# Optimization experiments

Measured on AMD Instinct MI355X. Metric: run time of the kernel, lower is better.

The kernel has to match this reference:

```python
import jax, jax.numpy as jnp
import numpy as np

B, L, H, D, TXT = 128, 512, 336, 256, 768
K, S, EMB = 16, 4, 128
H_SCALE = 0.15
EPS, ITERS = 0.05, 30
ALPHA, BETA = 1.0, 0.5
GW, TAU = 0.5, 0.07
LMB_MSE, LMB_COT, LMB_DELTA, LMB_ENT, LMB_TV = 1.0, 0.1, 0.1, 0.01, 0.01


def setup_inputs() -> dict:
    key = jax.random.key(0)
    ks = jax.random.split(key, 12)
    def xav(k, shape):
        return jax.random.normal(k, shape, jnp.float32) / np.sqrt(shape[0]).astype(np.float32)
    inp = {}
    inp['y_res'] = jax.random.normal(ks[0], (B, H, D), jnp.float32)
    inp['text_emb'] = jax.random.normal(ks[1], (B, TXT), jnp.float32)
    inp['enc_out'] = jax.random.normal(ks[2], (B, L, D), jnp.float32)
    inp['y_future'] = jax.random.normal(ks[3], (B, H, D), jnp.float32)
    inp['perm'] = jax.random.permutation(ks[4], EMB)
    inp['W_t2k'] = xav(ks[5], (TXT, K * (3 + S))); inp['b_t2k'] = jnp.zeros((K * (3 + S),), jnp.float32)
    inp['W_kemb'] = xav(ks[6], (H, EMB)); inp['b_kemb'] = jnp.zeros((EMB,), jnp.float32)
    inp['W_tir'] = xav(ks[7], (1, D)); inp['b_tir'] = jnp.zeros((D,), jnp.float32)
    inp['var_proj'] = jnp.ones((D,), jnp.float32)
    inp['W_g1'] = xav(ks[8], (2 * D + TXT, 512)); inp['b_g1'] = jnp.zeros((512,), jnp.float32)
    inp['W_g2'] = xav(ks[9], (512, D)); inp['b_g2'] = jnp.zeros((D,), jnp.float32)
    inp['W_fp'] = xav(ks[10], (3 * D, EMB)); inp['b_fp'] = jnp.zeros((EMB,), jnp.float32)
    return inp


def _text2kernels(text_emb, W, b):
    # text -> K temporal kernels: mixture of S shape bases with learned mu/sigma/amp
    raw = (text_emb @ W + b).reshape(-1, K, 3 + S)
    mu = jax.nn.sigmoid(raw[..., 0])                       # [B,K] center in [0,1]
    sig = jax.nn.softplus(raw[..., 1]) * H_SCALE + 1e-3     # [B,K] width
    amp = jax.nn.softplus(raw[..., 2])                      # [B,K]
    shape_w = jax.nn.softmax(raw[..., 3:], axis=-1)         # [B,K,S]
    t = (jnp.arange(H, dtype=text_emb.dtype) + 0.5) / H     # [H]
    z = (t[None, None, :] - mu[..., None]) / sig[..., None]  # [B,K,H]
    az = jnp.abs(z)
    in_supp = (az <= 1.0).astype(z.dtype)
    basis = jnp.stack([
        jnp.exp(-0.5 * z * z),
        jnp.exp(-az),
        jnp.maximum(1.0 - az, 0.0),
        0.5 * (1.0 + jnp.cos(jnp.pi * jnp.clip(z, -1.0, 1.0))) * in_supp,
    ], axis=-1)                                             # [B,K,H,S]
    kappa = amp[..., None] * jnp.einsum('bkhs,bks->bkh', basis, shape_w)
    return kappa, mu, shape_w


def _future_proj(y, W, b):
    # concat(y, first diff, second diff) -> linear, in_dim = 3*D
    d1 = jnp.diff(y, axis=1, prepend=y[:, :1])
    d2 = jnp.diff(d1, axis=1, prepend=d1[:, :1])
    return jnp.concatenate([y, d1, d2], axis=-1) @ W + b    # [B,H,EMB]


def _l2n(x):
    return x / (jnp.linalg.norm(x, axis=-1, keepdims=True) + 1e-8)


def _causal_cost(k_emb, f_pos, mu):
    cossim = jnp.einsum('bkd,bhd->bkh', _l2n(k_emb), _l2n(f_pos))
    t = (jnp.arange(H, dtype=k_emb.dtype) + 0.5) / H
    causal = jnp.maximum(mu[:, :, None] - t[None, None, :], 0.0)  # effect-before-cause penalty
    return ALPHA * (1.0 - cossim) + BETA * causal            # [B,K,H]


def _sinkhorn(C, r, c):
    Kmat = jnp.exp(-C / EPS)
    def body(i, uv):
        u, v = uv
        u = r / (jnp.einsum('bkh,bh->bk', Kmat, v) + 1e-9)
        v = c / (jnp.einsum('bkh,bk->bh', Kmat, u) + 1e-9)
        return (u, v)
    u, v = jax.lax.fori_loop(0, ITERS, body, (jnp.ones_like(r), jnp.ones_like(c)))
    return u[:, :, None] * Kmat * v[:, None, :]              # [B,K,H]


def _delta_contrastive(k_emb, f_pos, Pi, negatives):
    w = Pi / (jnp.sum(Pi, axis=-1, keepdims=True) + 1e-9)    # transport-weighted aggregation
    kn = _l2n(k_emb)
    def sim(f):
        return jnp.einsum('bkd,bkd->bk', kn, _l2n(jnp.einsum('bkh,bhd->bkd', w, f)))
    logits = jnp.stack([sim(f_pos)] + [sim(f) for f in negatives], axis=-1) / TAU  # [B,K,1+neg]
    return -jnp.mean(jax.nn.log_softmax(logits, axis=-1)[..., 0])


def reference(y_res, text_emb, enc_out, y_future, perm, W_t2k, b_t2k, W_kemb, b_kemb,
              W_tir, b_tir, var_proj, W_g1, b_g1, W_g2, b_g2, W_fp, b_fp):
    # --- text-induced response ---
    kappa, mu, shape_w = _text2kernels(text_emb, W_t2k, b_t2k)   # [B,K,H]
    y_tir_scalar = kappa.sum(axis=1)                             # [B,H]
    # --- gated fusion ---
    y_tir = (y_tir_scalar[..., None] @ W_tir + b_tir) * var_proj[None, None, :]  # [B,H,D]
    ts_global = enc_out.mean(axis=1)                             # [B,D]
    gate_in = jnp.concatenate([ts_global, text_emb, jnp.broadcast_to(var_proj[None, :], (y_res.shape[0], D))], axis=-1)
    gate = jax.nn.sigmoid(jax.nn.relu(gate_in @ W_g1 + b_g1) @ W_g2 + b_g2)[:, None, :]  # [B,1,D]
    y_hat = y_res + GW * gate * (y_tir - y_res)
    # --- aux losses ---
    k_emb = kappa @ W_kemb + b_kemb                              # [B,K,EMB]
    f_pos = _future_proj(y_future, W_fp, b_fp)                   # [B,H,EMB]
    C = _causal_cost(k_emb, f_pos, mu)
    r = jax.lax.stop_gradient(kappa.sum(-1) + 1e-6)
    r = r / r.sum(axis=-1, keepdims=True)
    c = jnp.full((C.shape[0], C.shape[2]), 1.0 / C.shape[2], C.dtype)
    Pi = _sinkhorn(C, r, c)
    shift = max(1, H // 6)
    f_neg1 = jnp.roll(f_pos, shift, axis=1)
    f_neg2 = f_pos[..., perm]
    loss_delta = _delta_contrastive(k_emb, f_pos, Pi, [f_neg1, f_neg2])
    loss_cot = jnp.mean(jnp.sum(C * Pi, axis=(1, 2)))
    sw = jnp.maximum(shape_w, 1e-8)
    loss_ent = -jnp.mean(jnp.sum(sw * jnp.log(sw), axis=-1))
    loss_tv = jnp.mean(jnp.abs(mu[:, 1:] - mu[:, :-1]))
    loss_mse = jnp.mean((y_hat - y_future) ** 2)
    return (LMB_MSE * loss_mse + LMB_COT * loss_cot + LMB_DELTA * loss_delta
            + LMB_ENT * loss_ent + LMB_TV * loss_tv)
```

## Files before the change

### kernel.cpp

```cpp
#include <hip/hip_runtime.h>
#include <math.h>

#define Bn   128
#define Ln   512
#define Hn   336
#define Dn   256
#define TXTn 768
#define Kn   16
#define EMBn 128
#define SHIFT 56
#define MSEB 1024
#define FROWS 48
#define FTILES 7
#define ASTRIDE 776

typedef __attribute__((ext_vector_type(8))) short short8;
typedef __attribute__((ext_vector_type(4))) float floatx4;

__device__ __forceinline__ float softplusf(float x){
  return fmaxf(x, 0.f) + log1pf(expf(-fabsf(x)));
}
__device__ __forceinline__ unsigned short f2bf(float x){
  unsigned int u = __float_as_uint(x);
  unsigned int r = (u + 0x7fffu + ((u >> 16) & 1u)) >> 16;
  return (unsigned short)r;
}
__device__ __forceinline__ float rcpf(float x){ return __builtin_amdgcn_rcpf(x); }
__device__ __forceinline__ float wsum(float x){
  x += __shfl_xor(x, 1);  x += __shfl_xor(x, 2);  x += __shfl_xor(x, 4);
  x += __shfl_xor(x, 8);  x += __shfl_xor(x, 16); x += __shfl_xor(x, 32);
  return x;
}

__global__ __launch_bounds__(256) void k_fused1(
    const float* __restrict__ text, const float* __restrict__ W, const float* __restrict__ bb,
    float* __restrict__ mu_o, float* __restrict__ kapT, float* __restrict__ rr_o,
    float* __restrict__ ytirs, float* __restrict__ part_ent, float* __restrict__ part_tv){
  int b = blockIdx.x, t = threadIdx.x;
  __shared__ float kapS[Kn*Hn];
  __shared__ float musL[Kn], sigL[Kn], ampL[Kn], shwL[Kn*4], entS[Kn], rrS[Kn];
  __shared__ float red[256];
  __shared__ float comb[112];
  __shared__ float totS;
  {
    int o = t & 127, half = t >> 7;
    if (o < 112){
      const float* tb = text + (size_t)b*TXTn + half*384;
      const float* Wb = W + (size_t)half*384*112 + o;
      float a0=0.f, a1=0.f, a2=0.f, a3=0.f;
      for (int i = 0; i < 384; i += 4){
        float4 x = *(const float4*)(tb + i);
        a0 += x.x*Wb[(i+0)*112]; a1 += x.y*Wb[(i+1)*112];
        a2 += x.z*Wb[(i+2)*112]; a3 += x.w*Wb[(i+3)*112];
      }
      red[half*112 + o] = (a0 + a1) + (a2 + a3);
    }
  }
  __syncthreads();
  if (t < 112) comb[t] = red[t] + red[112 + t] + bb[t];
  __syncthreads();
  if (t < Kn){
    float r0 = comb[t*7+0], r1 = comb[t*7+1], r2 = comb[t*7+2];
    float mu  = 1.f/(1.f+expf(-r0));
    float sig = softplusf(r1)*0.15f + 1e-3f;
    float amp = softplusf(r2);
    float s0 = comb[t*7+3], s1 = comb[t*7+4], s2 = comb[t*7+5], s3 = comb[t*7+6];
    float m = fmaxf(fmaxf(s0,s1), fmaxf(s2,s3));
    float e0 = expf(s0-m), e1 = expf(s1-m), e2 = expf(s2-m), e3 = expf(s3-m);
    float inv = 1.f/(e0+e1+e2+e3);
    float w0 = e0*inv, w1 = e1*inv, w2 = e2*inv, w3 = e3*inv;
    musL[t] = mu; sigL[t] = sig; ampL[t] = amp;
    shwL[t*4+0] = w0; shwL[t*4+1] = w1; shwL[t*4+2] = w2; shwL[t*4+3] = w3;
    mu_o[b*Kn + t] = mu;
    float ent = 0.f, sw;
    sw = fmaxf(w0,1e-8f); ent += sw*logf(sw);
    sw = fmaxf(w1,1e-8f); ent += sw*logf(sw);
    sw = fmaxf(w2,1e-8f); ent += sw*logf(sw);
    sw = fmaxf(w3,1e-8f); ent += sw*logf(sw);
    entS[t] = ent;
  }
  __syncthreads();
  for (int p = t; p < Kn*Hn; p += 256){
    int k = p/Hn, h = p - k*Hn;
    float mu = musL[k], sig = sigL[k], amp = ampL[k];
    float w0 = shwL[k*4+0], w1 = shwL[k*4+1], w2 = shwL[k*4+2], w3 = shwL[k*4+3];
    float tt = (h + 0.5f)/(float)Hn;
    float z  = (tt - mu)/sig;
    float az = fabsf(z);
    float b0 = expf(-0.5f*z*z);
    float b1 = expf(-az);
    float b2 = fmaxf(1.f-az, 0.f);
    float zc = fminf(fmaxf(z,-1.f),1.f);
    float b3 = (az <= 1.f) ? 0.5f*(1.f+cosf(3.14159265358979f*zc)) : 0.f;
    kapS[p] = amp*(w0*b0 + w1*b1 + w2*b2 + w3*b3);
  }
  __syncthreads();
  for (int q = t; q < Kn*Hn; q += 256){
    int h = q >> 4, k = q & 15;
    kapT[((size_t)b*Hn + h)*Kn + k] = kapS[k*Hn + h];
  }
  {
    int k = t >> 4, j16 = t & 15;
    float s = 0.f;
    for (int h = j16; h < Hn; h += 16) s += kapS[k*Hn + h];
    red[t] = s;
  }
  __syncthreads();
  if (t < Kn){
    float s = 0.f;
    for (int j = 0; j < 16; ++j) s += red[t*16 + j];
    rrS[t] = s + 1e-6f;
  }
  __syncthreads();
  if (t == 0){
    float tot = 0.f, tv = 0.f, es = 0.f;
    for (int k = 0; k < Kn; ++k) tot += rrS[k];
    for (int k = 1; k < Kn; ++k) tv += fabsf(musL[k]-musL[k-1]);
    for (int k = 0; k < Kn; ++k) es += entS[k];
    totS = tot; part_tv[b] = tv; part_ent[b] = es;
  }
  __syncthreads();
  if (t < Kn) rr_o[b*Kn + t] = rrS[t]/totS;
  for (int h = t; h < Hn; h += 256){
    float s = 0.f;
    #pragma unroll
    for (int k = 0; k < Kn; ++k) s += kapS[k*Hn + h];
    ytirs[b*Hn + h] = s;
  }
}

__global__ __launch_bounds__(128) void k_kemb1(const float* __restrict__ kapT,
    const float* __restrict__ W, float* __restrict__ kp){
  int blk = blockIdx.x;
  int b = blk >> 3, oc = blk & 7;
  int e = threadIdx.x;
  float acc[Kn];
  #pragma unroll
  for (int k = 0; k < Kn; ++k) acc[k] = 0.f;
  const float* kb = kapT + (size_t)b*Hn*Kn;
  int h0 = oc*42, h1 = h0 + 42;
  for (int h = h0; h < h1; ++h){
    float wv = W[h*EMBn + e];
    const float4* kr = (const float4*)(kb + h*Kn);
    float4 c0 = kr[0], c1 = kr[1], c2 = kr[2], c3 = kr[3];
    acc[0]  += c0.x*wv; acc[1]  += c0.y*wv; acc[2]  += c0.z*wv; acc[3]  += c0.w*wv;
    acc[4]  += c1.x*wv; acc[5]  += c1.y*wv; acc[6]  += c1.z*wv; acc[7]  += c1.w*wv;
    acc[8]  += c2.x*wv; acc[9]  += c2.y*wv; acc[10] += c2.z*wv; acc[11] += c2.w*wv;
    acc[12] += c3.x*wv; acc[13] += c3.y*wv; acc[14] += c3.z*wv; acc[15] += c3.w*wv;
  }
  float* kpb = kp + ((size_t)blk*Kn)*EMBn + e;
  #pragma unroll
  for (int k = 0; k < Kn; ++k) kpb[(size_t)k*EMBn] = acc[k];
}

__global__ __launch_bounds__(256) void k_kemb2(const float* __restrict__ kp,
    const float* __restrict__ bb, float* __restrict__ kn_o){
  int b = blockIdx.x, t = threadIdx.x;
  __shared__ float kS[Kn*EMBn];
  __shared__ float r2[256];
  __shared__ float invS[Kn];
  for (int j = t; j < Kn*EMBn; j += 256){
    int e = j & 127;
    float s = bb[e];
    const float* p = kp + (size_t)b*8*Kn*EMBn + j;
    #pragma unroll
    for (int oc = 0; oc < 8; ++oc) s += p[(size_t)oc*Kn*EMBn];
    kS[j] = s;
  }
  __syncthreads();
  {
    int k = t & 15, g = t >> 4;
    float s = 0.f;
    for (int e = g; e < EMBn; e += 16){ float v = kS[k*EMBn + e]; s += v*v; }
    r2[g*Kn + k] = s;
  }
  __syncthreads();
  if (t < Kn){
    float s = 0.f;
    for (int g = 0; g < 16; ++g) s += r2[g*Kn + t];
    invS[t] = 1.f/(sqrtf(s) + 1e-8f);
  }
  __syncthreads();
  for (int j = t; j < Kn*EMBn; j += 256)
    kn_o[(size_t)b*Kn*EMBn + j] = kS[j]*invS[j >> 7];
}

__global__ void k_wprep(const float* __restrict__ W, unsigned short* __restrict__ Bsw){
  int tid = blockIdx.x*256 + threadIdx.x;
  int k = tid >> 7, n = tid & 127;
  int kt = k >> 5, kr = k & 31, quad = kr >> 3, j = kr & 7;
  int c = n >> 4, ln = n & 15;
  int lane = quad*16 + ln;
  int dst = ((kt*8 + c)*64 + lane)*8 + j;
  Bsw[dst] = f2bf(W[k*128 + n]);
}

__global__ __launch_bounds__(256) void k_encmean(const float* __restrict__ enc,
                                                 float* __restrict__ psum){
  int blk = blockIdx.x;
  int b = blk >> 3, p = blk & 7;
  int t = threadIdx.x;
  int d4 = t & 63, rg = t >> 6;
  const float4* e4 = (const float4*)(enc + (size_t)b*Ln*Dn);
  float4 s = make_float4(0.f,0.f,0.f,0.f);
  for (int l = p + 8*rg; l < Ln; l += 32){
    float4 v = e4[(size_t)l*64 + d4];
    s.x += v.x; s.y += v.y; s.z += v.z; s.w += v.w;
  }
  __shared__ float4 red[256];
  red[t] = s;
  __syncthreads();
  if (rg == 0){
    float4 o = red[d4];
    #pragma unroll
    for (int r = 1; r < 4; ++r){
      float4 v = red[r*64 + d4];
      o.x += v.x; o.y += v.y; o.z += v.z; o.w += v.w;
    }
    ((float4*)(psum + ((size_t)b*8 + p)*Dn))[d4] = o;
  }
}

__global__ __launch_bounds__(256) void k_gmlp1(const float* __restrict__ psum,
    const float* __restrict__ text, const float* __restrict__ vp,
    const float* __restrict__ W1, float* __restrict__ hidp){
  int bt = blockIdx.x >> 5, hc = (blockIdx.x >> 2) & 7, ks = blockIdx.x & 3;
  int t = threadIdx.x;
  __shared__ float inS[4][320];
  for (int j = t; j < 4*320; j += 256){
    int bi = j / 320, jj = j - bi*320;
    int gi = ks*320 + jj;
    int b = bt*4 + bi;
    float vsl;
    if (gi < Dn){
      float s = 0.f;
      for (int p = 0; p < 8; ++p) s += psum[((size_t)b*8 + p)*Dn + gi];
      vsl = s * (1.f/(float)Ln);
    } else if (gi < Dn + TXTn){
      vsl = text[(size_t)b*TXTn + (gi - Dn)];
    } else {
      vsl = vp[gi - Dn - TXTn];
    }
    inS[bi][jj] = vsl;
  }
  __syncthreads();
  int h = t & 63, bi = t >> 6;
  int hidx = hc*64 + h;
  const float* Wb = W1 + (size_t)(ks*320)*512 + hidx;
  float a0 = 0.f, a1 = 0.f, a2 = 0.f, a3 = 0.f;
  const float4* in4 = (const float4*)inS[bi];
  for (int i = 0; i < 320; i += 4){
    float4 x = in4[i >> 2];
    a0 += x.x*Wb[(size_t)(i+0)*512]; a1 += x.y*Wb[(size_t)(i+1)*512];
    a2 += x.z*Wb[(size_t)(i+2)*512]; a3 += x.w*Wb[(size_t)(i+3)*512];
  }
  hidp[((size_t)ks*Bn + bt*4 + bi)*512 + hidx] = (a0 + a1) + (a2 + a3);
}

__global__ __launch_bounds__(256) void k_gmlp2(const float* __restrict__ hidp,
    const float* __restrict__ b1, const float* __restrict__ W2,
    const float* __restrict__ b2, float* __restrict__ gate_o){
  int bt = blockIdx.x >> 3, dc = blockIdx.x & 7;
  int t = threadIdx.x;
  __shared__ float hS[4][512];
  __shared__ float pS[8][4][32];
  for (int j = t; j < 4*512; j += 256){
    int bi = j >> 9, i = j & 511;
    size_t bidx = (size_t)(bt*4 + bi)*512 + i;
    float s = hidp[bidx] + hidp[(size_t)Bn*512 + bidx]
            + hidp[(size_t)2*Bn*512 + bidx] + hidp[(size_t)3*Bn*512 + bidx];
    hS[bi][i] = fmaxf(s + b1[i], 0.f);
  }
  __syncthreads();
  {
    int dl = t & 31, ig = t >> 5;
    int d  = dc*32 + dl;
    float a0=0.f, a1=0.f, a2=0.f, a3=0.f;
    int i0 = ig*64;
    for (int i = i0; i < i0 + 64; ++i){
      float wv = W2[(size_t)i*Dn + d];
      a0 += hS[0][i]*wv; a1 += hS[1][i]*wv;
      a2 += hS[2][i]*wv; a3 += hS[3][i]*wv;
    }
    pS[ig][0][dl] = a0; pS[ig][1][dl] = a1;
    pS[ig][2][dl] = a2; pS[ig][3][dl] = a3;
  }
  __syncthreads();
  if (t < 128){
    int bi = t >> 5, dl = t & 31;
    float s = 0.f;
    #pragma unroll
    for (int g = 0; g < 8; ++g) s += pS[g][bi][dl];
    s += b2[dc*32 + dl];
    gate_o[(size_t)(bt*4 + bi)*Dn + dc*32 + dl] = 1.f/(1.f + expf(-s));
  }
}

__global__ __launch_bounds__(256) void k_fposm(const float* __restrict__ yf,
    const unsigned short* __restrict__ Bsw, const float* __restrict__ bb,
    float* __restrict__ fpos, float* __restrict__ finv){
  int b = blockIdx.x / FTILES, tile = blockIdx.x % FTILES;
  int t = threadIdx.x;
  int h0 = tile*FROWS;
  __shared__ unsigned short yS[FROWS*ASTRIDE];
  __shared__ float rsq[4][FROWS];
  const float* yb = yf + (size_t)b*Hn*Dn;

  #pragma unroll
  for (int u = 0; u < 12; ++u){
    int unit = t + 256*u;
    int r = unit >> 6, d4 = unit & 63;
    int h = h0 + r;
    int hm1 = h-1 < 0 ? 0 : h-1;
    int hm2 = h-2 < 0 ? 0 : h-2;
    float4 y   = *(const float4*)(yb + (size_t)h  *Dn + d4*4);
    float4 ym1 = *(const float4*)(yb + (size_t)hm1*Dn + d4*4);
    float4 ym2 = *(const float4*)(yb + (size_t)hm2*Dn + d4*4);
    float4 d1 = make_float4(y.x-ym1.x, y.y-ym1.y, y.z-ym1.z, y.w-ym1.w);
    float4 d2 = make_float4(y.x-2.f*ym1.x+ym2.x, y.y-2.f*ym1.y+ym2.y,
                            y.z-2.f*ym1.z+ym2.z, y.w-2.f*ym1.w+ym2.w);
    union { unsigned short u16[4]; uint2 v; } p;
    unsigned short* base = &yS[r*ASTRIDE + d4*4];
    p.u16[0]=f2bf(y.x);  p.u16[1]=f2bf(y.y);  p.u16[2]=f2bf(y.z);  p.u16[3]=f2bf(y.w);
    *(uint2*)(base)        = p.v;
    p.u16[0]=f2bf(d1.x); p.u16[1]=f2bf(d1.y); p.u16[2]=f2bf(d1.z); p.u16[3]=f2bf(d1.w);
    *(uint2*)(base + 256)  = p.v;
    p.u16[0]=f2bf(d2.x); p.u16[1]=f2bf(d2.y); p.u16[2]=f2bf(d2.z); p.u16[3]=f2bf(d2.w);
    *(uint2*)(base + 512)  = p.v;
  }
  __syncthreads();

  int wv   = __builtin_amdgcn_readfirstlane(t >> 6);
  int lane = t & 63, quad = lane >> 4, ln = lane & 15;
  int c0 = wv*2;
  floatx4 acc[3][2];
  #pragma unroll
  for (int i = 0; i < 3; ++i){
    acc[i][0] = (floatx4){0.f,0.f,0.f,0.f};
    acc[i][1] = (floatx4){0.f,0.f,0.f,0.f};
  }
  #pragma unroll
  for (int kt = 0; kt < 24; ++kt){
    int aoff = kt*32 + quad*8;
    short8 a0 = *(const short8*)&yS[( 0 + ln)*ASTRIDE + aoff];
    short8 a1 = *(const short8*)&yS[(16 + ln)*ASTRIDE + aoff];
    short8 a2 = *(const short8*)&yS[(32 + ln)*ASTRIDE + aoff];
    short8 b0 = *(const short8*)&Bsw[((kt*8 + c0  )*64 + lane)*8];
    short8 b1 = *(const short8*)&Bsw[((kt*8 + c0+1)*64 + lane)*8];
    acc[0][0] = __builtin_amdgcn_mfma_f32_16x16x32_bf16(a0, b0, acc[0][0], 0, 0, 0);
    acc[0][1] = __builtin_amdgcn_mfma_f32_16x16x32_bf16(a0, b1, acc[0][1], 0, 0, 0);
    acc[1][0] = __builtin_amdgcn_mfma_f32_16x16x32_bf16(a1, b0, acc[1][0], 0, 0, 0);
    acc[1][1] = __builtin_amdgcn_mfma_f32_16x16x32_bf16(a1, b1, acc[1][1], 0, 0, 0);
    acc[2][0] = __builtin_amdgcn_mfma_f32_16x16x32_bf16(a2, b0, acc[2][0], 0, 0, 0);
    acc[2][1] = __builtin_amdgcn_mfma_f32_16x16x32_bf16(a2, b1, acc[2][1], 0, 0, 0);
  }

  float bias0 = bb[c0*16 + ln], bias1 = bb[(c0+1)*16 + ln];
  #pragma unroll
  for (int rt = 0; rt < 3; ++rt){
    #pragma unroll
    for (int reg = 0; reg < 4; ++reg){
      int lrow = rt*16 + quad*4 + reg;
      size_t row = (size_t)b*Hn + h0 + lrow;
      float v0 = acc[rt][0][reg] + bias0;
      float v1 = acc[rt][1][reg] + bias1;
      fpos[row*EMBn + c0*16 + ln]     = v0;
      fpos[row*EMBn + (c0+1)*16 + ln] = v1;
      float sq = v0*v0 + v1*v1;
      sq += __shfl_xor(sq, 1); sq += __shfl_xor(sq, 2);
      sq += __shfl_xor(sq, 4); sq += __shfl_xor(sq, 8);
      if (ln == 0) rsq[wv][lrow] = sq;
    }
  }
  __syncthreads();
  if (t < FROWS){
    float s = rsq[0][t] + rsq[1][t] + rsq[2][t] + rsq[3][t];
    finv[(size_t)b*Hn + h0 + t] = 1.f/(sqrtf(s) + 1e-8f);
  }
}

__global__ void k_mse(const float* __restrict__ yres, const float* __restrict__ yfut,
                      const float* __restrict__ gate, const float* __restrict__ ytirs,
                      const float* __restrict__ Wt, const float* __restrict__ bt,
                      const float* __restrict__ vp, float* __restrict__ part_mse){
  const long long total = (long long)Bn*Hn*Dn;
  long long tid = blockIdx.x*(long long)blockDim.x + threadIdx.x;
  long long nth = gridDim.x*(long long)blockDim.x;
  float part = 0.f;
  for (long long i4 = tid; i4*4 < total; i4 += nth){
    long long base = i4*4;
    int b = (int)(base/((long long)Hn*Dn));
    int rem = (int)(base - (long long)b*Hn*Dn);
    int h = rem/Dn, d = rem - h*Dn;
    float4 yr = *(const float4*)(yres + base);
    float4 yv = *(const float4*)(yfut + base);
    float4 g  = *(const float4*)(gate + (size_t)b*Dn + d);
    float4 wt = *(const float4*)(Wt + d);
    float4 bv = *(const float4*)(bt + d);
    float4 vv = *(const float4*)(vp + d);
    float ys = ytirs[b*Hn + h];
    float yt, yh, e;
    yt = (ys*wt.x + bv.x)*vv.x; yh = yr.x + 0.5f*g.x*(yt-yr.x); e = yh-yv.x; part += e*e;
    yt = (ys*wt.y + bv.y)*vv.y; yh = yr.y + 0.5f*g.y*(yt-yr.y); e = yh-yv.y; part += e*e;
    yt = (ys*wt.z + bv.z)*vv.z; yh = yr.z + 0.5f*g.z*(yt-yr.z); e = yh-yv.z; part += e*e;
    yt = (ys*wt.w + bv.w)*vv.w; yh = yr.w + 0.5f*g.w*(yt-yr.w); e = yh-yv.w; part += e*e;
  }
  __shared__ float red[256];
  red[threadIdx.x] = part; __syncthreads();
  for (int s = 128; s > 0; s >>= 1){
    if (threadIdx.x < s) red[threadIdx.x] += red[threadIdx.x + s];
    __syncthreads();
  }
  if (threadIdx.x == 0) part_mse[blockIdx.x] = red[0];
}

__global__ __launch_bounds__(256) void k_cost(const float* __restrict__ kn,
    const float* __restrict__ fpos, const float* __restrict__ finv,
    const float* __restrict__ mu_i, float* __restrict__ Km_g){
  int b = blockIdx.x >> 2, q = blockIdx.x & 3;
  int t = threadIdx.x;
  __shared__ float knS[Kn*132];
  __shared__ float musS[Kn];
  for (int j = t; j < Kn*EMBn; j += 256){
    int k = j >> 7, e = j & 127;
    knS[k*132 + e] = kn[(size_t)b*Kn*EMBn + j];
  }
  if (t < Kn) musS[t] = mu_i[b*Kn + t];
  __syncthreads();
  const int H0 = q*84;
  for (int p = t; p < Kn*84; p += 256){
    int k = p & 15, h = H0 + (p >> 4);
    const float4* f4 = (const float4*)(fpos + ((size_t)b*Hn + h)*EMBn);
    const float4* k4 = (const float4*)(knS + k*132);
    float s = 0.f;
    #pragma unroll 8
    for (int i = 0; i < EMBn/4; ++i){
      float4 a = k4[i], f = f4[i];
      s += a.x*f.x + a.y*f.y + a.z*f.z + a.w*f.w;
    }
    float cs = s*finv[b*Hn + h];
    float th = (h + 0.5f)/(float)Hn;
    float c  = (1.f - cs) + 0.5f*fmaxf(musS[k] - th, 0.f);
    Km_g[(size_t)b*Kn*Hn + k*Hn + h] = expf(-20.f*c);
  }
}

__global__ __launch_bounds__(128) void k_sink1w(const float* __restrict__ rr,
    float* KmwT, float* __restrict__ part_cot){
  int b = blockIdx.x, t = threadIdx.x;
  int l = t & 63;
  float* Kb = KmwT + (size_t)b*Kn*Hn;
  int ks = ((l&1)<<3) | ((l&2)<<1) | ((l&4)>>1) | ((l&8)>>3);
  __shared__ float ws[128];
  float km[16][3];
  #pragma unroll
  for (int m = 0; m < 16; ++m){
    const float* rowp = Kb + (size_t)(ks ^ m)*Hn;
    #pragma unroll
    for (int c = 0; c < 3; ++c){
      int h = 128*c + t;
      km[m][c] = (h < Hn) ? rowp[h] : 0.f;
    }
  }
  float rrl = rr[b*Kn + ks];
  float v[3];
  v[0] = 1.f; v[1] = 1.f; v[2] = 1.f;
  float w[16];
  for (int it = 0; it < 30; ++it){
    float p[16];
    #pragma unroll
    for (int m = 0; m < 16; ++m)
      p[m] = km[m][0]*v[0] + km[m][1]*v[1] + km[m][2]*v[2];
    #pragma unroll
    for (int m = 0; m < 8; ++m) p[m] += __shfl_xor(p[m+8], 1);
    #pragma unroll
    for (int m = 0; m < 4; ++m) p[m] += __shfl_xor(p[m+4], 2);
    #pragma unroll
    for (int m = 0; m < 2; ++m) p[m] += __shfl_xor(p[m+2], 4);
    p[0] += __shfl_xor(p[1], 8);
    p[0] += __shfl_xor(p[0], 16);
    p[0] += __shfl_xor(p[0], 32);
    ws[t] = p[0];
    __syncthreads();
    float ptot = ws[l] + ws[64 + l];
    __syncthreads();
    float ul = rrl * rcpf(ptot + 1e-9f);
    w[0] = ul;
    w[1] = __shfl_xor(w[0], 8);
    w[2] = __shfl_xor(w[0], 4); w[3] = __shfl_xor(w[1], 4);
    #pragma unroll
    for (int j = 0; j < 4; ++j) w[4+j] = __shfl_xor(w[j], 2);
    #pragma unroll
    for (int j = 0; j < 8; ++j) w[8+j] = __shfl_xor(w[j], 1);
    #pragma unroll
    for (int c = 0; c < 3; ++c){
      float s0 = 0.f, s1 = 0.f;
      #pragma unroll
      for (int m = 0; m < 8; ++m){ s0 += km[m][c]*w[m]; s1 += km[m+8][c]*w[m+8]; }
      v[c] = (1.f/(float)Hn) * rcpf(s0 + s1 + 1e-9f);
    }
  }
  float q[16];
  #pragma unroll
  for (int m = 0; m < 16; ++m)
    q[m] = km[m][0]*v[0] + km[m][1]*v[1] + km[m][2]*v[2];
  #pragma unroll
  for (int m = 0; m < 8; ++m) q[m] += __shfl_xor(q[m+8], 1);
  #pragma unroll
  for (int m = 0; m < 4; ++m) q[m] += __shfl_xor(q[m+4], 2);
  #pragma unroll
  for (int m = 0; m < 2; ++m) q[m] += __shfl_xor(q[m+2], 4);
  q[0] += __shfl_xor(q[1], 8);
  q[0] += __shfl_xor(q[0], 16);
  q[0] += __shfl_xor(q[0], 32);
  ws[t] = q[0];
  __syncthreads();
  float qtot = ws[l] + ws[64 + l];
  __syncthreads();
  float tt[16];
  tt[0] = qtot;
  tt[1] = __shfl_xor(tt[0], 8);
  tt[2] = __shfl_xor(tt[0], 4); tt[3] = __shfl_xor(tt[1], 4);
  #pragma unroll
  for (int j = 0; j < 4; ++j) tt[4+j] = __shfl_xor(tt[j], 2);
  #pragma unroll
  for (int j = 0; j < 8; ++j) tt[8+j] = __shfl_xor(tt[j], 1);
  float cot = 0.f;
  #pragma unroll
  for (int m = 0; m < 16; ++m){
    float rsinv = rcpf(w[m]*tt[m] + 1e-9f);
    float* rowp = Kb + (size_t)(ks ^ m)*Hn;
    #pragma unroll
    for (int c = 0; c < 3; ++c){
      int h = 128*c + t;
      if (h < Hn){
        float Pi = w[m]*km[m][c]*v[c];
        cot += (-0.05f)*logf(km[m][c])*Pi;
        rowp[h] = Pi*rsinv;
      }
    }
  }
  cot = wsum(cot);
  ws[t] = cot;
  __syncthreads();
  if (t == 0) part_cot[b] = ws[0] + ws[64];
}

__global__ __launch_bounds__(256) void k_agg(const float* __restrict__ kn,
    const float* __restrict__ fpos, const float* __restrict__ wT,
    const int* __restrict__ perm, float* __restrict__ part_del4){
  int b = blockIdx.x >> 2, kg = blockIdx.x & 3;
  int t = threadIdx.x;
  __shared__ float wTl[Hn*4];
  __shared__ float apH[2][4*EMBn];
  __shared__ float a1H[2][4*EMBn];
  __shared__ int permS[EMBn];
  __shared__ float redW[4];
  if (t < EMBn) permS[t] = perm[t];
  for (int j = t; j < 4*Hn; j += 256){
    int k = j & 3, h = j >> 2;
    wTl[h*4 + k] = wT[(size_t)b*Kn*Hn + (size_t)(kg*4 + k)*Hn + h];
  }
  __syncthreads();

  {
    int e = t & 127, jh = t >> 7;
    float ap[4], a1[4];
    #pragma unroll
    for (int j = 0; j < 4; ++j){ ap[j] = 0.f; a1[j] = 0.f; }
    const float* fb = fpos + (size_t)b*Hn*EMBn + e;
    int hh0 = jh*168, hh1 = hh0 + 168;
    for (int h = hh0; h < hh1; ++h){
      float fv = fb[(size_t)h*EMBn];
      int h1 = h + SHIFT; if (h1 >= Hn) h1 -= Hn;
      float4 wA = *(const float4*)&wTl[h *4];
      float4 wB = *(const float4*)&wTl[h1*4];
      ap[0] += wA.x*fv; ap[1] += wA.y*fv; ap[2] += wA.z*fv; ap[3] += wA.w*fv;
      a1[0] += wB.x*fv; a1[1] += wB.y*fv; a1[2] += wB.z*fv; a1[3] += wB.w*fv;
    }
    #pragma unroll
    for (int j = 0; j < 4; ++j){
      apH[jh][j*EMBn + e] = ap[j];
      a1H[jh][j*EMBn + e] = a1[j];
    }
  }
  __syncthreads();
  for (int j = t; j < 4*EMBn; j += 256){
    apH[0][j] += apH[1][j];
    a1H[0][j] += a1H[1][j];
  }
  __syncthreads();

  int wave = t >> 6, lane = t & 63;
  {
    int kl = wave;
    int k  = kg*4 + kl;
    float sp = 0.f, s1 = 0.f, s2 = 0.f, np = 0.f, n1 = 0.f;
    for (int e = lane; e < EMBn; e += 64){
      float kne = kn[((size_t)b*Kn + k)*EMBn + e];
      float a  = apH[0][kl*EMBn + e];
      float c1 = a1H[0][kl*EMBn + e];
      sp += kne*a; s1 += kne*c1;
      s2 += kne*apH[0][kl*EMBn + permS[e]];
      np += a*a; n1 += c1*c1;
    }
    for (int o = 32; o; o >>= 1){
      sp += __shfl_down(sp, o); s1 += __shfl_down(s1, o); s2 += __shfl_down(s2, o);
      np += __shfl_down(np, o); n1 += __shfl_down(n1, o);
    }
    if (lane == 0){
      float ip  = 1.f/(sqrtf(np) + 1e-8f);
      float i1v = 1.f/(sqrtf(n1) + 1e-8f);
      const float ti = 1.f/0.07f;
      float l0 = sp*ip*ti, l1 = s1*i1v*ti, l2 = s2*ip*ti;
      float m = fmaxf(l0, fmaxf(l1, l2));
      float lse = m + logf(expf(l0-m) + expf(l1-m) + expf(l2-m));
      redW[wave] = lse - l0;
    }
  }
  __syncthreads();
  if (t == 0) part_del4[(size_t)b*4 + kg] = redW[0] + redW[1] + redW[2] + redW[3];
}

__global__ void k_final(const float* __restrict__ part_mse, const float* __restrict__ part_cot,
                        const float* __restrict__ part_del4, const float* __restrict__ part_ent,
                        const float* __restrict__ part_tv, float* __restrict__ out){
  int t = threadIdx.x;
  __shared__ double sred[256];
  double m = 0.0;
  for (int i = t; i < MSEB; i += 256) m += (double)part_mse[i];
  double o4 = 0.0;
  if (t < Bn){
    double del = (double)part_del4[4*t] + (double)part_del4[4*t + 1]
               + (double)part_del4[4*t + 2] + (double)part_del4[4*t + 3];
    o4 = 0.1*(double)part_cot[t] + (0.1/(double)Kn)*del
       - (0.01/(double)Kn)*(double)part_ent[t] + (0.01/(double)(Kn-1))*(double)part_tv[t];
  }
  sred[t] = m/((double)Bn*Hn*Dn) + o4/(double)Bn;
  __syncthreads();
  for (int s = 128; s > 0; s >>= 1){ if (t < s) sred[t] += sred[t+s]; __syncthreads(); }
  if (t == 0) out[0] = (float)sred[0];
}

extern "C" void kernel_launch(void* const* d_in, const int* in_sizes, int n_in,
                              void* d_out, int out_size, void* d_ws, size_t ws_size,
                              hipStream_t stream) {
  const float* y_res  = (const float*)d_in[0];
  const float* text   = (const float*)d_in[1];
  const float* enc    = (const float*)d_in[2];
  const float* yfut   = (const float*)d_in[3];
  const int*   perm   = (const int*)  d_in[4];
  const float* W_t2k  = (const float*)d_in[5];
  const float* b_t2k  = (const float*)d_in[6];
  const float* W_kemb = (const float*)d_in[7];
  const float* b_kemb = (const float*)d_in[8];
  const float* W_tir  = (const float*)d_in[9];
  const float* b_tir  = (const float*)d_in[10];
  const float* vproj  = (const float*)d_in[11];
  const float* W_g1   = (const float*)d_in[12];
  const float* b_g1   = (const float*)d_in[13];
  const float* W_g2   = (const float*)d_in[14];
  const float* b_g2   = (const float*)d_in[15];
  const float* W_fp   = (const float*)d_in[16];
  const float* b_fp   = (const float*)d_in[17];

  float* F = (float*)d_ws;
  float* mu_w   = F;
  float* rr_w   = F + 2048;
  float* ytr_w  = F + 4096;
  float* kapT_w = F + 47104;
  float* kn_w   = F + 735232;
  float* gate_w = F + 997376;
  float* fp_w   = F + 1030144;
  float* fi_w   = F + 6535168;
  float* pmse_w = F + 6578176;
  float* pcot_w = F + 6579200;
  float* pent_w = F + 6579456;
  float* ptv_w  = F + 6579584;
  unsigned short* Bsw_w = (unsigned short*)kapT_w;
  float* KmwT_w = kapT_w;
  float* kp_w   = fp_w;
  float* psum_w = fp_w;
  float* hidp_w = fp_w + 262144;
  float* pdel4_w = gate_w;

  k_fused1 <<<Bn, 256, 0, stream>>>(text, W_t2k, b_t2k, mu_w, kapT_w, rr_w, ytr_w, pent_w, ptv_w);
  k_kemb1  <<<Bn*8, 128, 0, stream>>>(kapT_w, W_kemb, kp_w);
  k_kemb2  <<<Bn, 256, 0, stream>>>(kp_w, b_kemb, kn_w);
  k_wprep  <<<384, 256, 0, stream>>>(W_fp, Bsw_w);
  k_encmean<<<Bn*8, 256, 0, stream>>>(enc, psum_w);
  k_gmlp1  <<<1024, 256, 0, stream>>>(psum_w, text, vproj, W_g1, hidp_w);
  k_gmlp2  <<<256, 256, 0, stream>>>(hidp_w, b_g1, W_g2, b_g2, gate_w);
  k_fposm  <<<Bn*FTILES, 256, 0, stream>>>(yfut, Bsw_w, b_fp, fp_w, fi_w);
  k_mse    <<<MSEB, 256, 0, stream>>>(y_res, yfut, gate_w, ytr_w, W_tir, b_tir, vproj, pmse_w);
  k_cost   <<<Bn*4, 256, 0, stream>>>(kn_w, fp_w, fi_w, mu_w, KmwT_w);
  k_sink1w <<<Bn, 128, 0, stream>>>(rr_w, KmwT_w, pcot_w);
  k_agg    <<<Bn*4, 256, 0, stream>>>(kn_w, fp_w, KmwT_w, perm, pdel4_w);
  k_final  <<<1, 256, 0, stream>>>(pmse_w, pcot_w, pdel4_w, pent_w, ptv_w, (float*)d_out);
}
```

Measured before the change: 346.0 us.

## Rewrite Sinkhorn kernel to stage cost matrix in shared memory

Replaces the register-resident Sinkhorn kernel, which used 128 threads with xor-shuffle transposes, with a 256-thread version that keeps the K×H kernel matrix and the u/v scaling vectors in shared memory. Each iteration computes the row sums with 16-lane shuffle reductions and the column sums with per-thread loops over K, separated by block barriers. The final normalisation now uses a per-row dot product. This trades register shuffles for LDS traffic and more __syncthreads per iteration, and the v-update leaves threads idle because only 336 columns are split across 256 threads.

```diff
diff --git a/kernel.cpp b/kernel.cpp
--- a/kernel.cpp
+++ b/kernel.cpp
@@ -445,105 +445,56 @@
   }
 }
 
-__global__ __launch_bounds__(128) void k_sink1w(const float* __restrict__ rr,
+__global__ __launch_bounds__(256) void k_sink(const float* __restrict__ rr,
     float* KmwT, float* __restrict__ part_cot){
   int b = blockIdx.x, t = threadIdx.x;
-  int l = t & 63;
   float* Kb = KmwT + (size_t)b*Kn*Hn;
-  int ks = ((l&1)<<3) | ((l&2)<<1) | ((l&4)>>1) | ((l&8)>>3);
-  __shared__ float ws[128];
-  float km[16][3];
-  #pragma unroll
-  for (int m = 0; m < 16; ++m){
-    const float* rowp = Kb + (size_t)(ks ^ m)*Hn;
-    #pragma unroll
-    for (int c = 0; c < 3; ++c){
-      int h = 128*c + t;
-      km[m][c] = (h < Hn) ? rowp[h] : 0.f;
-    }
-  }
-  float rrl = rr[b*Kn + ks];
-  float v[3];
-  v[0] = 1.f; v[1] = 1.f; v[2] = 1.f;
-  float w[16];
+  __shared__ float KmS[Kn*Hn];
+  __shared__ float uS[Kn], vS[Hn], dotS[Kn], rrS[Kn];
+  __shared__ float redc[4];
+  for (int j = t; j < Kn*Hn; j += 256) KmS[j] = Kb[j];
+  for (int h = t; h < Hn; h += 256) vS[h] = 1.f;
+  if (t < Kn) rrS[t] = rr[b*Kn + t];
+  __syncthreads();
+  const int kk = t >> 4, hl = t & 15;
   for (int it = 0; it < 30; ++it){
-    float p[16];
-    #pragma unroll
-    for (int m = 0; m < 16; ++m)
-      p[m] = km[m][0]*v[0] + km[m][1]*v[1] + km[m][2]*v[2];
-    #pragma unroll
-    for (int m = 0; m < 8; ++m) p[m] += __shfl_xor(p[m+8], 1);
-    #pragma unroll
-    for (int m = 0; m < 4; ++m) p[m] += __shfl_xor(p[m+4], 2);
-    #pragma unroll
-    for (int m = 0; m < 2; ++m) p[m] += __shfl_xor(p[m+2], 4);
-    p[0] += __shfl_xor(p[1], 8);
-    p[0] += __shfl_xor(p[0], 16);
-    p[0] += __shfl_xor(p[0], 32);
-    ws[t] = p[0];
+    float s = 0.f;
+    for (int h = hl; h < Hn; h += 16) s += KmS[kk*Hn + h]*vS[h];
+    s += __shfl_xor(s, 1); s += __shfl_xor(s, 2);
+    s += __shfl_xor(s, 4); s += __shfl_xor(s, 8);
+    if (hl == 0) uS[kk] = rrS[kk]*rcpf(s + 1e-9f);
     __syncthreads();
-    float ptot = ws[l] + ws[64 + l];
+    for (int h = t; h < Hn; h += 256){
+      float sv = 0.f;
+      #pragma unroll
+      for (int k = 0; k < Kn; ++k) sv += KmS[k*Hn + h]*uS[k];
+      vS[h] = (1.f/(float)Hn)*rcpf(sv + 1e-9f);
+    }
     __syncthreads();
-    float ul = rrl * rcpf(ptot + 1e-9f);
-    w[0] = ul;
-    w[1] = __shfl_xor(w[0], 8);
-    w[2] = __shfl_xor(w[0], 4); w[3] = __shfl_xor(w[1], 4);
-    #pragma unroll
-    for (int j = 0; j < 4; ++j) w[4+j] = __shfl_xor(w[j], 2);
-    #pragma unroll
-    for (int j = 0; j < 8; ++j) w[8+j] = __shfl_xor(w[j], 1);
-    #pragma unroll
-    for (int c = 0; c < 3; ++c){
-      float s0 = 0.f, s1 = 0.f;
-      #pragma unroll
-      for (int m = 0; m < 8; ++m){ s0 += km[m][c]*w[m]; s1 += km[m+8][c]*w[m+8]; }
-      v[c] = (1.f/(float)Hn) * rcpf(s0 + s1 + 1e-9f);
-    }
-  }
-  float q[16];
-  #pragma unroll
-  for (int m = 0; m < 16; ++m)
-    q[m] = km[m][0]*v[0] + km[m][1]*v[1] + km[m][2]*v[2];
-  #pragma unroll
-  for (int m = 0; m < 8; ++m) q[m] += __shfl_xor(q[m+8], 1);
-  #pragma unroll
-  for (int m = 0; m < 4; ++m) q[m] += __shfl_xor(q[m+4], 2);
-  #pragma unroll
-  for (int m = 0; m < 2; ++m) q[m] += __shfl_xor(q[m+2], 4);
-  q[0] += __shfl_xor(q[1], 8);
-  q[0] += __shfl_xor(q[0], 16);
-  q[0] += __shfl_xor(q[0], 32);
-  ws[t] = q[0];
-  __syncthreads();
-  float qtot = ws[l] + ws[64 + l];
-  __syncthreads();
-  float tt[16];
-  tt[0] = qtot;
-  tt[1] = __shfl_xor(tt[0], 8);
-  tt[2] = __shfl_xor(tt[0], 4); tt[3] = __shfl_xor(tt[1], 4);
-  #pragma unroll
-  for (int j = 0; j < 4; ++j) tt[4+j] = __shfl_xor(tt[j], 2);
-  #pragma unroll
-  for (int j = 0; j < 8; ++j) tt[8+j] = __shfl_xor(tt[j], 1);
+  }
+  {
+    float s = 0.f;
+    for (int h = hl; h < Hn; h += 16) s += KmS[kk*Hn + h]*vS[h];
+    s += __shfl_xor(s, 1); s += __shfl_xor(s, 2);
+    s += __shfl_xor(s, 4); s += __shfl_xor(s, 8);
+    if (hl == 0) dotS[kk] = s;
+  }
+  __syncthreads();
   float cot = 0.f;
   #pragma unroll
-  for (int m = 0; m < 16; ++m){
-    float rsinv = rcpf(w[m]*tt[m] + 1e-9f);
-    float* rowp = Kb + (size_t)(ks ^ m)*Hn;
-    #pragma unroll
-    for (int c = 0; c < 3; ++c){
-      int h = 128*c + t;
-      if (h < Hn){
-        float Pi = w[m]*km[m][c]*v[c];
-        cot += (-0.05f)*logf(km[m][c])*Pi;
-        rowp[h] = Pi*rsinv;
-      }
+  for (int k = 0; k < Kn; ++k){
+    float uk = uS[k], dinv = rcpf(dotS[k] + 1e-30f);
+    for (int h = t; h < Hn; h += 256){
+      float kmv = KmS[k*Hn + h];
+      float Pi = uk*kmv*vS[h];
+      cot += (-0.05f)*logf(kmv)*Pi;
+      Kb[k*Hn + h] = kmv*vS[h]*dinv;
     }
   }
   cot = wsum(cot);
-  ws[t] = cot;
-  __syncthreads();
-  if (t == 0) part_cot[b] = ws[0] + ws[64];
+  if ((t & 63) == 0) redc[t >> 6] = cot;
+  __syncthreads();
+  if (t == 0) part_cot[b] = redc[0] + redc[1] + redc[2] + redc[3];
 }
 
 __global__ __launch_bounds__(256) void k_agg(const float* __restrict__ kn,
@@ -694,7 +645,7 @@
   k_fposm  <<<Bn*FTILES, 256, 0, stream>>>(yfut, Bsw_w, b_fp, fp_w, fi_w);
   k_mse    <<<MSEB, 256, 0, stream>>>(y_res, yfut, gate_w, ytr_w, W_tir, b_tir, vproj, pmse_w);
   k_cost   <<<Bn*4, 256, 0, stream>>>(kn_w, fp_w, fi_w, mu_w, KmwT_w);
-  k_sink1w <<<Bn, 128, 0, stream>>>(rr_w, KmwT_w, pcot_w);
+  k_sink   <<<Bn, 256, 0, stream>>>(rr_w, KmwT_w, pcot_w);
   k_agg    <<<Bn*4, 256, 0, stream>>>(kn_w, fp_w, KmwT_w, perm, pdel4_w);
   k_final  <<<1, 256, 0, stream>>>(pmse_w, pcot_w, pdel4_w, pent_w, ptv_w, (float*)d_out);
 }
```

After: 368.5 us. 6.5% more time.
